# Kernel optimization log

Measured on AMD Instinct MI355X. Metric: run time of the kernel, lower is better.

## Reference

```python
import jax, jax.numpy as jnp
import numpy as np

ALPHA = 0.2  # LeakyReLU negative slope


def setup_inputs() -> dict:
    key = jax.random.key(0)
    k1, k2, k3 = jax.random.split(key, 3)
    B, N, D_in, D_out = 16, 2048, 128, 128
    x = jax.random.normal(k1, (B, N, D_in), dtype=jnp.float32)
    # xavier-uniform-ish scale for params
    W = jax.random.normal(k2, (D_in, D_out), dtype=jnp.float32) * (1.414 / np.sqrt(D_in + D_out))
    a = jax.random.normal(k3, (2 * D_out, 1), dtype=jnp.float32) * (1.414 / np.sqrt(2 * D_out + 1))
    return {"x": x, "W": W, "a": a}


def reference(x, W, a):
    # h: (B, N, D)
    h = jnp.matmul(x, W)
    D = h.shape[-1]
    # a = [a1; a2]; e[b,i,j] = leakyrelu(a1 . h_i + a2 . h_j)
    a1 = a[:D, 0]   # (D,)
    a2 = a[D:, 0]   # (D,)
    s1 = jnp.einsum('bnd,d->bn', h, a1)  # (B, N) source term
    s2 = jnp.einsum('bnd,d->bn', h, a2)  # (B, N) target term
    e = jax.nn.leaky_relu(s1[:, :, None] + s2[:, None, :], negative_slope=ALPHA)  # (B, N, N)
    attention = jax.nn.softmax(e, axis=2)
    h_prime = jnp.matmul(attention, h)  # (B, N, D)
    return jax.nn.relu(h_prime)  # concat=True -> relu
```

## Files before the change

kernel.cpp:

```cpp
#include <hip/hip_runtime.h>
#include <hip/hip_bf16.h>
#include <cstddef>

#define GAT_B 16
#define GAT_N 2048
#define GAT_D 128
#define GAT_ROWS (GAT_B * GAT_N)
#define CH 256
#define CL 8
#define GAT_ALPHA 0.2f

typedef __attribute__((ext_vector_type(8))) short short8v;
typedef __attribute__((ext_vector_type(4))) float f32x4;

__device__ __forceinline__ void cvt_hilo(float x, unsigned short& hi, unsigned short& lo) {
  union { float f; unsigned u; } a;
  a.f = x;
  hi = (unsigned short)(a.u >> 16);
  union { unsigned u; float f; } b;
  b.u = (unsigned)hi << 16;
  union { float f; unsigned u; } c;
  c.f = x - b.f;
  lo = (unsigned short)(c.u >> 16);
}

__global__ __launch_bounds__(256) void k0_wfrag(const float* __restrict__ W,
                                                unsigned short* __restrict__ WfH,
                                                unsigned short* __restrict__ WfL) {
  const int t = blockIdx.x * 256 + threadIdx.x;
  const int n = t & 127, g = (t >> 7) & 3, ks = t >> 9;
  short8v vh, vl;
#pragma unroll
  for (int j = 0; j < 8; ++j) {
    const int k = ks * 32 + g * 8 + j;
    unsigned short hi, lo;
    cvt_hilo(W[k * 128 + n], hi, lo);
    vh[j] = (short)hi;
    vl[j] = (short)lo;
  }
  *(short8v*)&WfH[t * 8] = vh;
  *(short8v*)&WfL[t * 8] = vl;
}

__global__ __launch_bounds__(256) void k1_gemm(const float* __restrict__ x,
                                               const unsigned short* __restrict__ WfHg,
                                               const unsigned short* __restrict__ WfLg,
                                               const float* __restrict__ aa,
                                               float* __restrict__ h,
                                               float* __restrict__ s1part,
                                               float* __restrict__ s2part) {
  __shared__ unsigned short xH[64 * 128];
  __shared__ unsigned short xL[64 * 128];
  const int tid = threadIdx.x;
  const int row0 = blockIdx.x * 64;

#pragma unroll
  for (int p = 0; p < 8; ++p) {
    const int row = p * 8 + (tid >> 5);
    const int f4 = tid & 31;
    const float4 v = ((const float4*)(x + (size_t)(row0 + row) * GAT_D))[f4];
    unsigned short h0, h1, h2, h3, l0, l1, l2, l3;
    cvt_hilo(v.x, h0, l0);
    cvt_hilo(v.y, h1, l1);
    cvt_hilo(v.z, h2, l2);
    cvt_hilo(v.w, h3, l3);
    const int slot = (f4 >> 1) ^ (row & 7);
    const int base = row * 128 + slot * 8 + (f4 & 1) * 4;
    *(ushort4*)&xH[base] = make_ushort4(h0, h1, h2, h3);
    *(ushort4*)&xL[base] = make_ushort4(l0, l1, l2, l3);
  }

  const int w = tid >> 6, l = tid & 63;
  const int wc0 = w * 32;
  const int g = l >> 4, c16 = l & 15;

  short8v bh[4][2], bl[4][2];
#pragma unroll
  for (int ks = 0; ks < 4; ++ks)
#pragma unroll
    for (int nt = 0; nt < 2; ++nt) {
      const int bi = ((ks * 4 + g) * 128 + wc0 + nt * 16 + c16) * 8;
      bh[ks][nt] = *(const short8v*)&WfHg[bi];
      bl[ks][nt] = *(const short8v*)&WfLg[bi];
    }

  __syncthreads();

  f32x4 acc[4][2];
#pragma unroll
  for (int mt = 0; mt < 4; ++mt)
#pragma unroll
    for (int nt = 0; nt < 2; ++nt) acc[mt][nt] = (f32x4)(0.f);

#pragma unroll
  for (int ks = 0; ks < 4; ++ks) {
    short8v ah[4], al[4];
#pragma unroll
    for (int mt = 0; mt < 4; ++mt) {
      const int row = mt * 16 + c16;
      const int ai = row * 128 + (((ks * 4 + g) ^ (row & 7)) * 8);
      ah[mt] = *(const short8v*)&xH[ai];
      al[mt] = *(const short8v*)&xL[ai];
    }
#pragma unroll
    for (int mt = 0; mt < 4; ++mt) {
#pragma unroll
      for (int nt = 0; nt < 2; ++nt) {
        acc[mt][nt] = __builtin_amdgcn_mfma_f32_16x16x32_bf16(ah[mt], bh[ks][nt], acc[mt][nt], 0, 0, 0);
        acc[mt][nt] = __builtin_amdgcn_mfma_f32_16x16x32_bf16(al[mt], bh[ks][nt], acc[mt][nt], 0, 0, 0);
        acc[mt][nt] = __builtin_amdgcn_mfma_f32_16x16x32_bf16(ah[mt], bl[ks][nt], acc[mt][nt], 0, 0, 0);
      }
    }
  }

#pragma unroll
  for (int mt = 0; mt < 4; ++mt)
#pragma unroll
    for (int nt = 0; nt < 2; ++nt)
#pragma unroll
      for (int j = 0; j < 4; ++j)
        h[(size_t)(row0 + mt * 16 + g * 4 + j) * GAT_D + wc0 + nt * 16 + c16] =
            acc[mt][nt][j];

  float a1v[2], a2v[2];
#pragma unroll
  for (int nt = 0; nt < 2; ++nt) {
    a1v[nt] = aa[wc0 + nt * 16 + c16];
    a2v[nt] = aa[128 + wc0 + nt * 16 + c16];
  }
#pragma unroll
  for (int mt = 0; mt < 4; ++mt) {
#pragma unroll
    for (int j = 0; j < 4; ++j) {
      float t1 = acc[mt][0][j] * a1v[0] + acc[mt][1][j] * a1v[1];
      float t2 = acc[mt][0][j] * a2v[0] + acc[mt][1][j] * a2v[1];
#pragma unroll
      for (int off = 1; off < 16; off <<= 1) {
        t1 += __shfl_xor(t1, off);
        t2 += __shfl_xor(t2, off);
      }
      if (c16 == 0) {
        const int row = row0 + mt * 16 + g * 4 + j;
        s1part[w * GAT_ROWS + row] = t1;
        s2part[w * GAT_ROWS + row] = t2;
      }
    }
  }
}

__global__ __launch_bounds__(1024) void k2_sort(const float* __restrict__ s1part,
                                                const float* __restrict__ s2part,
                                                float* __restrict__ s2s,
                                                int* __restrict__ idxs,
                                                float* __restrict__ s1s,
                                                int* __restrict__ rids,
                                                float* __restrict__ wA,
                                                float* __restrict__ wP,
                                                float* __restrict__ preDenA,
                                                float* __restrict__ sufDenP) {
  __shared__ float v[2048];
  __shared__ int id[2048];
  __shared__ float wtotA[16];
  __shared__ float wtotP[16];
  const int tid = threadIdx.x;
  const int b = blockIdx.x >> 1;
  const int half = blockIdx.x & 1;
  const int i0 = tid, i1 = tid + 1024;
  const float* src = (half == 0) ? s2part : s1part;
  {
    const int r0 = b * GAT_N + i0, r1 = b * GAT_N + i1;
    float v0 = src[r0] + src[GAT_ROWS + r0] + src[2 * GAT_ROWS + r0] + src[3 * GAT_ROWS + r0];
    float v1 = src[r1] + src[GAT_ROWS + r1] + src[2 * GAT_ROWS + r1] + src[3 * GAT_ROWS + r1];
    if (half == 1) {
      v0 = -v0;
      v1 = -v1;
    }
    v[i0] = v0;
    v[i1] = v1;
  }
  id[i0] = i0;
  id[i1] = i1;
  for (int k = 2; k <= 2048; k <<= 1) {
    for (int j = k >> 1; j > 0; j >>= 1) {
      __syncthreads();
      const int i = ((tid & ~(j - 1)) << 1) | (tid & (j - 1));
      const int ixj = i | j;
      const bool up = (i & k) == 0;
      const float va = v[i], vb = v[ixj];
      if (up ? (va > vb) : (va < vb)) {
        v[i] = vb;
        v[ixj] = va;
        const int ta = id[i];
        id[i] = id[ixj];
        id[ixj] = ta;
      }
    }
  }
  __syncthreads();
  if (half == 1) {
    s1s[b * GAT_N + i0] = -v[i0];
    s1s[b * GAT_N + i1] = -v[i1];
    rids[b * GAT_N + i0] = id[i0];
    rids[b * GAT_N + i1] = id[i1];
    return;
  }
  s2s[b * GAT_N + i0] = v[i0];
  s2s[b * GAT_N + i1] = v[i1];
  idxs[b * GAT_N + i0] = id[i0];
  idxs[b * GAT_N + i1] = id[i1];

  const int lane = tid & 63, w = tid >> 6;
  const float aL = __expf(GAT_ALPHA * v[2 * tid]);
  const float aR = __expf(GAT_ALPHA * v[2 * tid + 1]);
  const float pL = __expf(v[2047 - 2 * tid]);
  const float pR = __expf(v[2046 - 2 * tid]);
  wA[b * GAT_N + 2 * tid] = aL;
  wA[b * GAT_N + 2 * tid + 1] = aR;
  wP[b * GAT_N + 2047 - 2 * tid] = pL;
  wP[b * GAT_N + 2046 - 2 * tid] = pR;
  float sA = aL + aR, sP = pL + pR;
#pragma unroll
  for (int off = 1; off < 64; off <<= 1) {
    const float tA = __shfl_up(sA, off);
    const float tP = __shfl_up(sP, off);
    if (lane >= off) {
      sA += tA;
      sP += tP;
    }
  }
  if (lane == 63) {
    wtotA[w] = sA;
    wtotP[w] = sP;
  }
  __syncthreads();
  float offA = 0.f, offP = 0.f;
  for (int ww = 0; ww < w; ++ww) {
    offA += wtotA[ww];
    offP += wtotP[ww];
  }
  const float inclA = offA + sA;
  const float inclP = offP + sP;
  preDenA[b * GAT_N + 2 * tid] = inclA - aR;
  preDenA[b * GAT_N + 2 * tid + 1] = inclA;
  sufDenP[b * GAT_N + 2047 - 2 * tid] = inclP - pR;
  sufDenP[b * GAT_N + 2046 - 2 * tid] = inclP;
}

__global__ __launch_bounds__(128) void k3_permute(const float* __restrict__ h,
                                                  const int* __restrict__ idxs,
                                                  const float* __restrict__ wA,
                                                  const float* __restrict__ wP,
                                                  float* __restrict__ hs,
                                                  float* __restrict__ partA,
                                                  float* __restrict__ partP) {
  const int b = blockIdx.x >> 7, cc = blockIdx.x & 127;
  const int d = threadIdx.x;
  const int* idxb = idxs + b * GAT_N;
  const float* hb = h + (size_t)b * GAT_N * GAT_D;
#pragma unroll
  for (int sub = 0; sub < 2; ++sub) {
    const int c = cc * 2 + sub;
    const int q0 = c * CL;
    float accA = 0.f, accP = 0.f;
#pragma unroll
    for (int qq = 0; qq < CL; ++qq) {
      const int q = q0 + qq;
      const int j = idxb[q];
      const float hv = hb[(size_t)j * GAT_D + d];
      hs[((size_t)b * GAT_N + q) * GAT_D + d] = hv;
      accA = fmaf(wA[b * GAT_N + q], hv, accA);
      accP = fmaf(wP[b * GAT_N + q], hv, accP);
    }
    partA[(b * CH + c) * GAT_D + d] = accA;
    partP[(b * CH + c) * GAT_D + d] = accP;
  }
}

__global__ __launch_bounds__(1024) void k3b_prep(const float* __restrict__ s1s,
                                                 const float* __restrict__ s2s,
                                                 const float* __restrict__ preDenA,
                                                 const float* __restrict__ sufDenP,
                                                 const float* __restrict__ partA,
                                                 const float* __restrict__ partP,
                                                 float* __restrict__ baseA,
                                                 float* __restrict__ baseP,
                                                 int* __restrict__ pArr,
                                                 float* __restrict__ c1,
                                                 float* __restrict__ c2) {
  __shared__ float totA[8][128];
  __shared__ float totP[8][128];
  __shared__ float sh[2048];
  const int b = blockIdx.x >> 1;
  const int role = blockIdx.x & 1;
  const int t = threadIdx.x;
  if (role == 0) {
    const int d = t & 127, g = t >> 7;
    const float* pA = partA + (size_t)(b * CH + g * 32) * GAT_D + d;
    const float* pP = partP + (size_t)(b * CH + g * 32) * GAT_D + d;
    float sA = 0.f, sP = 0.f;
#pragma unroll 8
    for (int i = 0; i < 32; ++i) {
      sA += pA[i * GAT_D];
      sP += pP[i * GAT_D];
    }
    totA[g][d] = sA;
    totP[g][d] = sP;
    __syncthreads();
    float offA = 0.f, offP = 0.f;
    for (int gg = 0; gg < g; ++gg) offA += totA[gg][d];
    for (int gg = g + 1; gg < 8; ++gg) offP += totP[gg][d];
    float run = offA;
#pragma unroll 8
    for (int i = 0; i < 32; ++i) {
      baseA[(size_t)(b * (CH + 1) + g * 32 + i) * GAT_D + d] = run;
      run += pA[i * GAT_D];
    }
    if (g == 7) baseA[(size_t)(b * (CH + 1) + CH) * GAT_D + d] = run;
    run = offP;
#pragma unroll 8
    for (int i = 31; i >= 0; --i) {
      baseP[(size_t)(b * CH + g * 32 + i) * GAT_D + d] = run;
      run += pP[i * GAT_D];
    }
  } else {
    sh[t] = s2s[b * GAT_N + t];
    sh[t + 1024] = s2s[b * GAT_N + t + 1024];
    __syncthreads();
#pragma unroll
    for (int rr = 0; rr < 2; ++rr) {
      const int j = t + rr * 1024;
      const float s1v = s1s[b * GAT_N + j];
      const float tt = -s1v;
      int lo = 0, hi = GAT_N;
      while (lo < hi) {
        const int mid = (lo + hi) >> 1;
        if (sh[mid] < tt)
          lo = mid + 1;
        else
          hi = mid;
      }
      const float e1 = __expf(s1v), e2 = __expf(GAT_ALPHA * s1v);
      float den = 0.f;
      if (lo < GAT_N) den += e1 * sufDenP[b * GAT_N + lo];
      if (lo > 0) den += e2 * preDenA[b * GAT_N + lo - 1];
      const float inv = 1.f / den;
      pArr[b * GAT_N + j] = lo;
      c1[b * GAT_N + j] = e1 * inv;
      c2[b * GAT_N + j] = e2 * inv;
    }
  }
}

__global__ __launch_bounds__(256) void k5_out(const float* __restrict__ hs,
                                              const float* __restrict__ wA,
                                              const float* __restrict__ wP,
                                              const float* __restrict__ baseA,
                                              const float* __restrict__ baseP,
                                              const int* __restrict__ pArr,
                                              const float* __restrict__ c1,
                                              const float* __restrict__ c2,
                                              const int* __restrict__ rids,
                                              float* __restrict__ out) {
  const int wave = threadIdx.x >> 6, lane = threadIdx.x & 63;
  const int j = blockIdx.x * 4 + wave;
  const int b = j >> 11;
  const int jr = b * GAT_N + (j & 2047);
  const int p = pArr[jr];
  const float cc1 = c1[jr], cc2 = c2[jr];
  const int rid = rids[jr];
  const float2* hs2 = (const float2*)(hs + (size_t)b * GAT_N * GAT_D);
  const float* wAb = wA + b * GAT_N;
  const float* wPb = wP + b * GAT_N;

  const int cA = p >> 3;
  float2 accA = ((const float2*)(baseA + (size_t)(b * (CH + 1) + cA) * GAT_D))[lane];
#pragma unroll 4
  for (int q = cA * CL; q < p; ++q) {
    const float w = wAb[q];
    const float2 hv = hs2[(size_t)q * 64 + lane];
    accA.x = fmaf(w, hv.x, accA.x);
    accA.y = fmaf(w, hv.y, accA.y);
  }

  const int pP = p < GAT_N ? p : GAT_N - 1;
  const int cP = pP >> 3;
  float2 accP = ((const float2*)(baseP + (size_t)(b * CH + cP) * GAT_D))[lane];
  const int qend = cP * CL + CL;
#pragma unroll 4
  for (int q = p; q < qend; ++q) {
    const float w = wPb[q];
    const float2 hv = hs2[(size_t)q * 64 + lane];
    accP.x = fmaf(w, hv.x, accP.x);
    accP.y = fmaf(w, hv.y, accP.y);
  }

  const float vx = cc2 * accA.x + cc1 * accP.x;
  const float vy = cc2 * accA.y + cc1 * accP.y;
  ((float2*)out)[(size_t)(b * GAT_N + rid) * 64 + lane] =
      make_float2(fmaxf(vx, 0.f), fmaxf(vy, 0.f));
}

extern "C" void kernel_launch(void* const* d_in, const int* in_sizes, int n_in,
                              void* d_out, int out_size, void* d_ws, size_t ws_size,
                              hipStream_t stream) {
  (void)in_sizes;
  (void)n_in;
  (void)out_size;
  (void)ws_size;
  const float* x = (const float*)d_in[0];
  const float* W = (const float*)d_in[1];
  const float* a = (const float*)d_in[2];
  float* out = (float*)d_out;
  float* wsf = (float*)d_ws;

  const size_t HN = (size_t)GAT_ROWS * GAT_D;
  size_t o = 0;
  float* s1part = wsf + o;   o += 4 * GAT_ROWS;
  float* s2part = wsf + o;   o += 4 * GAT_ROWS;
  float* s2s = wsf + o;      o += GAT_ROWS;
  int* idxs = (int*)(wsf + o); o += GAT_ROWS;
  float* s1s = wsf + o;      o += GAT_ROWS;
  int* rids = (int*)(wsf + o); o += GAT_ROWS;
  float* preDenA = wsf + o;  o += GAT_ROWS;
  float* sufDenP = wsf + o;  o += GAT_ROWS;
  float* wAr = wsf + o;      o += GAT_ROWS;
  float* wPr = wsf + o;      o += GAT_ROWS;
  int* pArr = (int*)(wsf + o); o += GAT_ROWS;
  float* c1 = wsf + o;       o += GAT_ROWS;
  float* c2 = wsf + o;       o += GAT_ROWS;
  float* partA = wsf + o;    o += (size_t)GAT_B * CH * GAT_D;
  float* partP = wsf + o;    o += (size_t)GAT_B * CH * GAT_D;
  float* baseA = wsf + o;    o += (size_t)GAT_B * (CH + 1) * GAT_D;
  float* baseP = wsf + o;    o += (size_t)GAT_B * CH * GAT_D;
  unsigned short* WfH = (unsigned short*)(wsf + o); o += 8192;
  unsigned short* WfL = (unsigned short*)(wsf + o); o += 8192;
  float* h = wsf + o;        o += HN;
  float* hs = wsf + o;       o += HN;

  k0_wfrag<<<8, 256, 0, stream>>>(W, WfH, WfL);
  k1_gemm<<<512, 256, 0, stream>>>(x, WfH, WfL, a, h, s1part, s2part);
  k2_sort<<<2 * GAT_B, 1024, 0, stream>>>(s1part, s2part, s2s, idxs, s1s, rids, wAr, wPr,
                                          preDenA, sufDenP);
  k3_permute<<<GAT_B * 128, 128, 0, stream>>>(h, idxs, wAr, wPr, hs, partA, partP);
  k3b_prep<<<2 * GAT_B, 1024, 0, stream>>>(s1s, s2s, preDenA, sufDenP, partA, partP,
                                           baseA, baseP, pArr, c1, c2);
  k5_out<<<GAT_ROWS / 4, 256, 0, stream>>>(hs, wAr, wPr, baseA, baseP, pArr, c1, c2,
                                           rids, out);
}
```

Before: 76.43 us.

## Drop s1 sort; binary-search unsorted s1 rows directly in sort kernel

Rows no longer need sorting by s1, because each row's split point can be found by binary search over the sorted s2 values no matter what order the rows are in. The s1 half of the sort kernel is removed, and the binary search plus normalisation constants move into the s2 sort block, which keeps the prefix denominators in shared memory. This removes a bitonic sort, several global intermediate arrays and the output scatter through rids, since output rows are now written in natural order. The cost is that the sort kernel runs half as many blocks and each does the search work serially after its sort, while the scan kernel keeps only the partial-sum role.

Measured after the change: 82.91 us. +8.5%, slower.

```diff
diff --git a/kernel.cpp b/kernel.cpp
--- a/kernel.cpp
+++ b/kernel.cpp
@@ -150,33 +150,27 @@
 
 __global__ __launch_bounds__(1024) void k2_sort(const float* __restrict__ s1part,
                                                 const float* __restrict__ s2part,
-                                                float* __restrict__ s2s,
                                                 int* __restrict__ idxs,
-                                                float* __restrict__ s1s,
-                                                int* __restrict__ rids,
                                                 float* __restrict__ wA,
                                                 float* __restrict__ wP,
-                                                float* __restrict__ preDenA,
-                                                float* __restrict__ sufDenP) {
+                                                int* __restrict__ pArr,
+                                                float* __restrict__ c1,
+                                                float* __restrict__ c2) {
   __shared__ float v[2048];
   __shared__ int id[2048];
+  __shared__ float denA[2048];
+  __shared__ float denP[2048];
   __shared__ float wtotA[16];
   __shared__ float wtotP[16];
   const int tid = threadIdx.x;
-  const int b = blockIdx.x >> 1;
-  const int half = blockIdx.x & 1;
+  const int b = blockIdx.x;
   const int i0 = tid, i1 = tid + 1024;
-  const float* src = (half == 0) ? s2part : s1part;
   {
     const int r0 = b * GAT_N + i0, r1 = b * GAT_N + i1;
-    float v0 = src[r0] + src[GAT_ROWS + r0] + src[2 * GAT_ROWS + r0] + src[3 * GAT_ROWS + r0];
-    float v1 = src[r1] + src[GAT_ROWS + r1] + src[2 * GAT_ROWS + r1] + src[3 * GAT_ROWS + r1];
-    if (half == 1) {
-      v0 = -v0;
-      v1 = -v1;
-    }
-    v[i0] = v0;
-    v[i1] = v1;
+    v[i0] = s2part[r0] + s2part[GAT_ROWS + r0] + s2part[2 * GAT_ROWS + r0] +
+            s2part[3 * GAT_ROWS + r0];
+    v[i1] = s2part[r1] + s2part[GAT_ROWS + r1] + s2part[2 * GAT_ROWS + r1] +
+            s2part[3 * GAT_ROWS + r1];
   }
   id[i0] = i0;
   id[i1] = i1;
@@ -197,15 +191,6 @@
     }
   }
   __syncthreads();
-  if (half == 1) {
-    s1s[b * GAT_N + i0] = -v[i0];
-    s1s[b * GAT_N + i1] = -v[i1];
-    rids[b * GAT_N + i0] = id[i0];
-    rids[b * GAT_N + i1] = id[i1];
-    return;
-  }
-  s2s[b * GAT_N + i0] = v[i0];
-  s2s[b * GAT_N + i1] = v[i1];
   idxs[b * GAT_N + i0] = id[i0];
   idxs[b * GAT_N + i1] = id[i1];
 
@@ -240,10 +225,36 @@
   }
   const float inclA = offA + sA;
   const float inclP = offP + sP;
-  preDenA[b * GAT_N + 2 * tid] = inclA - aR;
-  preDenA[b * GAT_N + 2 * tid + 1] = inclA;
-  sufDenP[b * GAT_N + 2047 - 2 * tid] = inclP - pR;
-  sufDenP[b * GAT_N + 2046 - 2 * tid] = inclP;
+  denA[2 * tid] = inclA - aR;
+  denA[2 * tid + 1] = inclA;
+  denP[2047 - 2 * tid] = inclP - pR;
+  denP[2046 - 2 * tid] = inclP;
+  __syncthreads();
+
+#pragma unroll
+  for (int rr = 0; rr < 2; ++rr) {
+    const int j = tid + rr * 1024;
+    const int r = b * GAT_N + j;
+    const float s1v = s1part[r] + s1part[GAT_ROWS + r] + s1part[2 * GAT_ROWS + r] +
+                      s1part[3 * GAT_ROWS + r];
+    const float tt = -s1v;
+    int lo = 0, hi = GAT_N;
+    while (lo < hi) {
+      const int mid = (lo + hi) >> 1;
+      if (v[mid] < tt)
+        lo = mid + 1;
+      else
+        hi = mid;
+    }
+    const float e1 = __expf(s1v), e2 = __expf(GAT_ALPHA * s1v);
+    float den = 0.f;
+    if (lo < GAT_N) den += e1 * denP[lo];
+    if (lo > 0) den += e2 * denA[lo - 1];
+    const float inv = 1.f / den;
+    pArr[r] = lo;
+    c1[r] = e1 * inv;
+    c2[r] = e2 * inv;
+  }
 }
 
 __global__ __launch_bounds__(128) void k3_permute(const float* __restrict__ h,
@@ -276,78 +287,41 @@
   }
 }
 
-__global__ __launch_bounds__(1024) void k3b_prep(const float* __restrict__ s1s,
-                                                 const float* __restrict__ s2s,
-                                                 const float* __restrict__ preDenA,
-                                                 const float* __restrict__ sufDenP,
-                                                 const float* __restrict__ partA,
+__global__ __launch_bounds__(1024) void k3b_scan(const float* __restrict__ partA,
                                                  const float* __restrict__ partP,
                                                  float* __restrict__ baseA,
-                                                 float* __restrict__ baseP,
-                                                 int* __restrict__ pArr,
-                                                 float* __restrict__ c1,
-                                                 float* __restrict__ c2) {
+                                                 float* __restrict__ baseP) {
   __shared__ float totA[8][128];
   __shared__ float totP[8][128];
-  __shared__ float sh[2048];
-  const int b = blockIdx.x >> 1;
-  const int role = blockIdx.x & 1;
+  const int b = blockIdx.x;
   const int t = threadIdx.x;
-  if (role == 0) {
-    const int d = t & 127, g = t >> 7;
-    const float* pA = partA + (size_t)(b * CH + g * 32) * GAT_D + d;
-    const float* pP = partP + (size_t)(b * CH + g * 32) * GAT_D + d;
-    float sA = 0.f, sP = 0.f;
+  const int d = t & 127, g = t >> 7;
+  const float* pA = partA + (size_t)(b * CH + g * 32) * GAT_D + d;
+  const float* pP = partP + (size_t)(b * CH + g * 32) * GAT_D + d;
+  float sA = 0.f, sP = 0.f;
 #pragma unroll 8
-    for (int i = 0; i < 32; ++i) {
-      sA += pA[i * GAT_D];
-      sP += pP[i * GAT_D];
-    }
-    totA[g][d] = sA;
-    totP[g][d] = sP;
-    __syncthreads();
-    float offA = 0.f, offP = 0.f;
-    for (int gg = 0; gg < g; ++gg) offA += totA[gg][d];
-    for (int gg = g + 1; gg < 8; ++gg) offP += totP[gg][d];
-    float run = offA;
+  for (int i = 0; i < 32; ++i) {
+    sA += pA[i * GAT_D];
+    sP += pP[i * GAT_D];
+  }
+  totA[g][d] = sA;
+  totP[g][d] = sP;
+  __syncthreads();
+  float offA = 0.f, offP = 0.f;
+  for (int gg = 0; gg < g; ++gg) offA += totA[gg][d];
+  for (int gg = g + 1; gg < 8; ++gg) offP += totP[gg][d];
+  float run = offA;
 #pragma unroll 8
-    for (int i = 0; i < 32; ++i) {
-      baseA[(size_t)(b * (CH + 1) + g * 32 + i) * GAT_D + d] = run;
-      run += pA[i * GAT_D];
-    }
-    if (g == 7) baseA[(size_t)(b * (CH + 1) + CH) * GAT_D + d] = run;
-    run = offP;
+  for (int i = 0; i < 32; ++i) {
+    baseA[(size_t)(b * (CH + 1) + g * 32 + i) * GAT_D + d] = run;
+    run += pA[i * GAT_D];
+  }
+  if (g == 7) baseA[(size_t)(b * (CH + 1) + CH) * GAT_D + d] = run;
+  run = offP;
 #pragma unroll 8
-    for (int i = 31; i >= 0; --i) {
-      baseP[(size_t)(b * CH + g * 32 + i) * GAT_D + d] = run;
-      run += pP[i * GAT_D];
-    }
-  } else {
-    sh[t] = s2s[b * GAT_N + t];
-    sh[t + 1024] = s2s[b * GAT_N + t + 1024];
-    __syncthreads();
-#pragma unroll
-    for (int rr = 0; rr < 2; ++rr) {
-      const int j = t + rr * 1024;
-      const float s1v = s1s[b * GAT_N + j];
-      const float tt = -s1v;
-      int lo = 0, hi = GAT_N;
-      while (lo < hi) {
-        const int mid = (lo + hi) >> 1;
-        if (sh[mid] < tt)
-          lo = mid + 1;
-        else
-          hi = mid;
-      }
-      const float e1 = __expf(s1v), e2 = __expf(GAT_ALPHA * s1v);
-      float den = 0.f;
-      if (lo < GAT_N) den += e1 * sufDenP[b * GAT_N + lo];
-      if (lo > 0) den += e2 * preDenA[b * GAT_N + lo - 1];
-      const float inv = 1.f / den;
-      pArr[b * GAT_N + j] = lo;
-      c1[b * GAT_N + j] = e1 * inv;
-      c2[b * GAT_N + j] = e2 * inv;
-    }
+  for (int i = 31; i >= 0; --i) {
+    baseP[(size_t)(b * CH + g * 32 + i) * GAT_D + d] = run;
+    run += pP[i * GAT_D];
   }
 }
 
@@ -359,15 +333,13 @@
                                               const int* __restrict__ pArr,
                                               const float* __restrict__ c1,
                                               const float* __restrict__ c2,
-                                              const int* __restrict__ rids,
                                               float* __restrict__ out) {
   const int wave = threadIdx.x >> 6, lane = threadIdx.x & 63;
   const int j = blockIdx.x * 4 + wave;
   const int b = j >> 11;
-  const int jr = b * GAT_N + (j & 2047);
+  const int jr = j;
   const int p = pArr[jr];
   const float cc1 = c1[jr], cc2 = c2[jr];
-  const int rid = rids[jr];
   const float2* hs2 = (const float2*)(hs + (size_t)b * GAT_N * GAT_D);
   const float* wAb = wA + b * GAT_N;
   const float* wPb = wP + b * GAT_N;
@@ -396,7 +368,7 @@
 
   const float vx = cc2 * accA.x + cc1 * accP.x;
   const float vy = cc2 * accA.y + cc1 * accP.y;
-  ((float2*)out)[(size_t)(b * GAT_N + rid) * 64 + lane] =
+  ((float2*)out)[(size_t)jr * 64 + lane] =
       make_float2(fmaxf(vx, 0.f), fmaxf(vy, 0.f));
 }
 
@@ -417,12 +389,7 @@
   size_t o = 0;
   float* s1part = wsf + o;   o += 4 * GAT_ROWS;
   float* s2part = wsf + o;   o += 4 * GAT_ROWS;
-  float* s2s = wsf + o;      o += GAT_ROWS;
   int* idxs = (int*)(wsf + o); o += GAT_ROWS;
-  float* s1s = wsf + o;      o += GAT_ROWS;
-  int* rids = (int*)(wsf + o); o += GAT_ROWS;
-  float* preDenA = wsf + o;  o += GAT_ROWS;
-  float* sufDenP = wsf + o;  o += GAT_ROWS;
   float* wAr = wsf + o;      o += GAT_ROWS;
   float* wPr = wsf + o;      o += GAT_ROWS;
   int* pArr = (int*)(wsf + o); o += GAT_ROWS;
@@ -439,11 +406,8 @@
 
   k0_wfrag<<<8, 256, 0, stream>>>(W, WfH, WfL);
   k1_gemm<<<512, 256, 0, stream>>>(x, WfH, WfL, a, h, s1part, s2part);
-  k2_sort<<<2 * GAT_B, 1024, 0, stream>>>(s1part, s2part, s2s, idxs, s1s, rids, wAr, wPr,
-                                          preDenA, sufDenP);
+  k2_sort<<<GAT_B, 1024, 0, stream>>>(s1part, s2part, idxs, wAr, wPr, pArr, c1, c2);
   k3_permute<<<GAT_B * 128, 128, 0, stream>>>(h, idxs, wAr, wPr, hs, partA, partP);
-  k3b_prep<<<2 * GAT_B, 1024, 0, stream>>>(s1s, s2s, preDenA, sufDenP, partA, partP,
-                                           baseA, baseP, pArr, c1, c2);
-  k5_out<<<GAT_ROWS / 4, 256, 0, stream>>>(hs, wAr, wPr, baseA, baseP, pArr, c1, c2,
-                                           rids, out);
-}
+  k3b_scan<<<GAT_B, 1024, 0, stream>>>(partA, partP, baseA, baseP);
+  k5_out<<<GAT_ROWS / 4, 256, 0, stream>>>(hs, wAr, wPr, baseA, baseP, pArr, c1, c2, out);
+}
```

## Do bitonic sort stages within a wavefront using register shuffles

Applied to the files above, without the earlier changes.

Replaces the shared-memory bitonic sort, which needed a block barrier at every compare-exchange step, with a hybrid. Each thread holds two adjacent elements in registers and resolves strides below 128 with __shfl_xor and in-register swaps. Only strides of 128 or more still go through shared memory with __syncthreads. This removes most barriers and LDS traffic in the sort kernel, but adds index tie-breaking and a register round trip per large stage.

Result: faster. 70.32 us (-8.0%).

```diff
diff --git a/kernel.cpp b/kernel.cpp
--- a/kernel.cpp
+++ b/kernel.cpp
@@ -178,25 +178,76 @@
     v[i0] = v0;
     v[i1] = v1;
   }
-  id[i0] = i0;
-  id[i1] = i1;
-  for (int k = 2; k <= 2048; k <<= 1) {
-    for (int j = k >> 1; j > 0; j >>= 1) {
-      __syncthreads();
+  __syncthreads();
+
+  const int lane = tid & 63;
+  const int e0 = ((tid >> 6) << 7) + lane * 2;
+  const int e1 = e0 + 1;
+  float va = v[e0], vb = v[e1];
+  int ida = e0, idb = e1;
+
+  auto lanex = [&](int k, int j) {
+    const int jl = j >> 1;
+    const bool dir = (e0 & k) == 0;
+    const bool lower = (lane & jl) == 0;
+    const bool keepMax = lower ^ dir;
+    {
+      const float ov = __shfl_xor(va, jl);
+      const int oid = __shfl_xor(ida, jl);
+      const bool ogt = (ov > va) || (ov == va && oid > ida);
+      if (ogt == keepMax) { va = ov; ida = oid; }
+    }
+    {
+      const float ov = __shfl_xor(vb, jl);
+      const int oid = __shfl_xor(idb, jl);
+      const bool ogt = (ov > vb) || (ov == vb && oid > idb);
+      if (ogt == keepMax) { vb = ov; idb = oid; }
+    }
+  };
+  auto pairx = [&](int k) {
+    const bool dir = (e0 & k) == 0;
+    const bool bgt = (vb > va) || (vb == va && idb > ida);
+    if (bgt != dir) {
+      const float tv = va; va = vb; vb = tv;
+      const int ti = ida; ida = idb; idb = ti;
+    }
+  };
+
+#pragma unroll
+  for (int k = 2; k <= 128; k <<= 1) {
+#pragma unroll
+    for (int j = k >> 1; j >= 2; j >>= 1) lanex(k, j);
+    pairx(k);
+  }
+  v[e0] = va; id[e0] = ida;
+  v[e1] = vb; id[e1] = idb;
+  __syncthreads();
+
+  for (int k = 256; k <= 2048; k <<= 1) {
+    for (int j = k >> 1; j >= 128; j >>= 1) {
       const int i = ((tid & ~(j - 1)) << 1) | (tid & (j - 1));
       const int ixj = i | j;
       const bool up = (i & k) == 0;
-      const float va = v[i], vb = v[ixj];
-      if (up ? (va > vb) : (va < vb)) {
-        v[i] = vb;
-        v[ixj] = va;
-        const int ta = id[i];
+      const float x0 = v[i], x1 = v[ixj];
+      if (up ? (x0 > x1) : (x0 < x1)) {
+        v[i] = x1;
+        v[ixj] = x0;
+        const int ti = id[i];
         id[i] = id[ixj];
-        id[ixj] = ta;
+        id[ixj] = ti;
       }
-    }
-  }
-  __syncthreads();
+      __syncthreads();
+    }
+    va = v[e0]; ida = id[e0];
+    vb = v[e1]; idb = id[e1];
+#pragma unroll
+    for (int j = 64; j >= 2; j >>= 1) lanex(k, j);
+    pairx(k);
+    v[e0] = va; id[e0] = ida;
+    v[e1] = vb; id[e1] = idb;
+    __syncthreads();
+  }
+
   if (half == 1) {
     s1s[b * GAT_N + i0] = -v[i0];
     s1s[b * GAT_N + i1] = -v[i1];
@@ -209,7 +260,7 @@
   idxs[b * GAT_N + i0] = id[i0];
   idxs[b * GAT_N + i1] = id[i1];
 
-  const int lane = tid & 63, w = tid >> 6;
+  const int w = tid >> 6;
   const float aL = __expf(GAT_ALPHA * v[2 * tid]);
   const float aR = __expf(GAT_ALPHA * v[2 * tid + 1]);
   const float pL = __expf(v[2047 - 2 * tid]);
```
